# Kernel optimization log

Measured on AMD Instinct MI355X. Metric: run time of the kernel, lower is better.

Reference implementation:

```python
import jax, jax.numpy as jnp
import numpy as np

B, T, C, H = 2048, 81, 128, 4
HD = C // H  # head dim = 32


def sudoku_mask():
    # att[i,j] = 0 if cells i,j share a row, column, or 3x3 block; else -inf.
    idx = np.arange(81)
    row, col = idx // 9, idx % 9
    block_a, block_b = col // 3, row // 3  # equality test matches original's swapped naming
    same = (row[:, None] == row[None, :]) | (col[:, None] == col[None, :]) | (
        (block_a[:, None] == block_a[None, :]) & (block_b[:, None] == block_b[None, :]))
    return jnp.asarray(np.where(same, 0.0, -np.inf), dtype=jnp.float32)


def setup_inputs() -> dict:
    key = jax.random.key(0)
    ks = jax.random.split(key, 7)
    s = 1.0 / np.sqrt(C)
    return {
        "x": jax.random.normal(ks[0], (B, T, C), jnp.float32),
        "key_value_states": jax.random.normal(ks[1], (B, T, C), jnp.float32),
        "Wq": jax.random.normal(ks[2], (C, C), jnp.float32) * s,
        "bq": jnp.zeros((C,), jnp.float32),
        "Wk": jax.random.normal(ks[3], (C, C), jnp.float32) * s,
        "bk": jnp.zeros((C,), jnp.float32),
        "Wv": jax.random.normal(ks[4], (C, C), jnp.float32) * s,
        "bv": jnp.zeros((C,), jnp.float32),
        "Wp": jax.random.normal(ks[5], (C, C), jnp.float32) * s,
        "bp": jnp.zeros((C,), jnp.float32),
    }


def reference(x, key_value_states, Wq, bq, Wk, bk, Wv, bv, Wp, bp):
    mask = sudoku_mask()  # [T, Te]
    # projections -> [B, H, T, HD]
    q = (x @ Wq + bq).reshape(B, T, H, HD).transpose(0, 2, 1, 3)
    k = (key_value_states @ Wk + bk).reshape(B, T, H, HD).transpose(0, 2, 1, 3)
    v = (key_value_states @ Wv + bv).reshape(B, T, H, HD).transpose(0, 2, 1, 3)
    att = jnp.einsum("bhqd,bhkd->bhqk", q, k) * (1.0 / np.sqrt(HD))
    att = att + mask  # broadcast over [B, H]
    att_to_check = att  # pre-softmax scores (the clone in torch)
    p = jax.nn.softmax(att, axis=-1)  # attn_drop is identity (p=0 / eval)
    y = jnp.einsum("bhqk,bhkd->bhqd", p, v)
    y = y.transpose(0, 2, 1, 3).reshape(B, T, C)
    y = y @ Wp + bp  # resid_drop is identity
    return (y, att_to_check)
```

## Files before the change

kernel.cpp:

```cpp
#include <hip/hip_runtime.h>
#include <math.h>

namespace {
constexpr int NB = 2048;
constexpr int TT = 81;
constexpr int CC = 128;
constexpr int NH = 4;
constexpr int HD = 32;
constexpr int BT  = TT * CC;
constexpr int ATTS = NH * TT * TT;
constexpr int MT = NB * TT / 64;
constexpr float SCALE = 0.17677669529663687f;
constexpr float MASKED = -1.0e30f;
}

__device__ __forceinline__ int swz(int row, int k) {
    return row * CC + (k ^ ((row & 7) << 2));
}

struct MaskTab { unsigned w[TT][4]; };
constexpr MaskTab make_mask() {
    MaskTab t{};
    for (int i = 0; i < TT; ++i) {
        const int ri = i / 9, ci = i % 9;
        for (int j = 0; j < TT; ++j) {
            const int rj = j / 9, cj = j % 9;
            const bool same = (ri == rj) || (ci == cj) ||
                              ((ri / 3 == rj / 3) && (ci / 3 == cj / 3));
            if (same) t.w[i][j >> 5] |= 1u << (j & 31);
        }
    }
    return t;
}
__device__ __constant__ MaskTab MASKT = make_mask();

__global__ __launch_bounds__(512, 6)
void qkv_gemm(const float* __restrict__ x, const float* __restrict__ kvs,
              const float* __restrict__ Wq, const float* __restrict__ bq,
              const float* __restrict__ Wk, const float* __restrict__ bk,
              const float* __restrict__ Wv, const float* __restrict__ bv,
              float* __restrict__ qk_region,
              float* __restrict__ v_region,
              size_t qk_stride)
{
    __shared__ float act[64 * CC];

    const int tid = threadIdx.x;
    const int sel = blockIdx.y;
    const float* W    = (sel == 0) ? Wq : (sel == 1) ? Wk : Wv;
    const float* bias = (sel == 0) ? bq : (sel == 1) ? bk : bv;
    const float* src  = (sel == 0) ? x  : kvs;
    const size_t gbase = (size_t)blockIdx.x * 64 * CC;

    for (int t = tid; t < 64 * CC / 4; t += 512) {
        const int row = t >> 5;
        const int k0  = (t & 31) << 2;
        *reinterpret_cast<float4*>(&act[swz(row, k0)]) =
            *reinterpret_cast<const float4*>(src + gbase + t * 4);
    }
    __syncthreads();

    const int lane = tid & 63;
    const int col0 = __builtin_amdgcn_readfirstlane(tid >> 6) << 4;
    const int m    = blockIdx.x * 64 + lane;
    const int bb   = m / TT;
    const int ii   = m - bb * TT;

    float acc[16];
    #pragma unroll
    for (int c = 0; c < 16; ++c) acc[c] = bias[col0 + c];

    for (int k4 = 0; k4 < 32; ++k4) {
        const float4 a = *reinterpret_cast<const float4*>(&act[swz(lane, k4 * 4)]);
        const float* wr = W + (size_t)(k4 * 4) * CC + col0;
        #pragma unroll
        for (int kk = 0; kk < 4; ++kk) {
            const float av = (kk == 0) ? a.x : (kk == 1) ? a.y
                           : (kk == 2) ? a.z : a.w;
            #pragma unroll
            for (int c4 = 0; c4 < 4; ++c4) {
                const float4 w =
                    *reinterpret_cast<const float4*>(wr + kk * CC + c4 * 4);
                acc[c4 * 4 + 0] = fmaf(av, w.x, acc[c4 * 4 + 0]);
                acc[c4 * 4 + 1] = fmaf(av, w.y, acc[c4 * 4 + 1]);
                acc[c4 * 4 + 2] = fmaf(av, w.z, acc[c4 * 4 + 2]);
                acc[c4 * 4 + 3] = fmaf(av, w.w, acc[c4 * 4 + 3]);
            }
        }
    }

    float* dst = (sel == 2)
        ? v_region  + (size_t)bb * BT + ii * CC + col0
        : qk_region + (size_t)bb * qk_stride + (size_t)sel * BT + ii * CC + col0;
    #pragma unroll
    for (int c4 = 0; c4 < 4; ++c4)
        reinterpret_cast<float4*>(dst)[c4] =
            make_float4(acc[c4*4+0], acc[c4*4+1], acc[c4*4+2], acc[c4*4+3]);
}

__global__ __launch_bounds__(256, 3)
void attn_head(const float* __restrict__ qk_ws,
               float* __restrict__ att_region,
               float* __restrict__ yv_region)
{
    __shared__ float Qh[TT * HD];
    __shared__ float Vh[TT * HD];
    __shared__ float Su[TT * TT];

    const int bh  = blockIdx.x;
    const int b   = bh >> 2;
    const int h   = bh & 3;
    const int tid = threadIdx.x;

    const float* qbase = qk_ws + (size_t)b * 2 * BT;
    const float* kbase = qbase + BT;
    float* vbase = yv_region + (size_t)b * BT;
    float* abase = att_region + (size_t)b * ATTS + (size_t)h * TT * TT;

    for (int t = tid; t < TT * 8; t += 256) {
        const int i  = t >> 3;
        const int c4 = (t & 7) << 2;
        const float4 qv = *reinterpret_cast<const float4*>(qbase + i * CC + h * HD + c4);
        const float4 vv = *reinterpret_cast<const float4*>(vbase + i * CC + h * HD + c4);
        const float4 kv = *reinterpret_cast<const float4*>(kbase + i * CC + h * HD + c4);
        *reinterpret_cast<float4*>(&Qh[i * HD + c4]) = qv;
        *reinterpret_cast<float4*>(&Vh[i * HD + c4]) = vv;
        Su[i * 33 + c4 + 0] = kv.x;
        Su[i * 33 + c4 + 1] = kv.y;
        Su[i * 33 + c4 + 2] = kv.z;
        Su[i * 33 + c4 + 3] = kv.w;
    }
    __syncthreads();

    const int io = tid / 41;
    const int jg = tid - io * 41;
    const bool sact = tid < 246;
    const int j0 = jg * 2;
    const int j1 = j0 + 1;
    const bool hasj1 = j1 < TT;
    const int j1r = hasj1 ? j1 : j0;

    float k0[HD], k1[HD];
    if (sact) {
        #pragma unroll
        for (int c = 0; c < HD; ++c) {
            k0[c] = Su[j0 * 33 + c];
            k1[c] = Su[j1r * 33 + c];
        }
    }
    __syncthreads();

    if (sact) {
        const int w0 = j0 >> 5, s0b = j0 & 31;
        const int w1 = j1 >> 5, s1b = j1 & 31;
        const int i0   = (io < 3) ? io * 14 : 42 + (io - 3) * 13;
        const int ilen = (io < 3) ? 14 : 13;
        for (int t = 0; t < ilen; ++t) {
            const int i = i0 + t;
            const float4* qf = reinterpret_cast<const float4*>(&Qh[i * HD]);
            float s0 = 0.f, s1 = 0.f;
            #pragma unroll
            for (int c4 = 0; c4 < 8; ++c4) {
                const float4 q4 = qf[c4];
                s0 = fmaf(q4.x, k0[c4*4+0], s0); s0 = fmaf(q4.y, k0[c4*4+1], s0);
                s0 = fmaf(q4.z, k0[c4*4+2], s0); s0 = fmaf(q4.w, k0[c4*4+3], s0);
                s1 = fmaf(q4.x, k1[c4*4+0], s1); s1 = fmaf(q4.y, k1[c4*4+1], s1);
                s1 = fmaf(q4.z, k1[c4*4+2], s1); s1 = fmaf(q4.w, k1[c4*4+3], s1);
            }
            const unsigned mw0 = MASKT.w[i][w0];
            Su[i * TT + j0] = ((mw0 >> s0b) & 1u) ? s0 * SCALE : MASKED;
            if (hasj1) {
                const unsigned mw1 = MASKT.w[i][w1];
                Su[i * TT + j1] = ((mw1 >> s1b) & 1u) ? s1 * SCALE : MASKED;
            }
        }
    }
    __syncthreads();

    for (int e = tid; e < TT * TT; e += 256)
        abase[e] = Su[e];

    if (tid < 2 * TT) {
        const int ph = tid / TT;
        const int pi = tid - ph * TT;
        const int d0 = ph * 16;
        const float* srow = &Su[pi * TT];

        float m0 = -INFINITY, m1 = -INFINITY, m2 = -INFINITY;
        for (int j = 0; j < TT; j += 3) {
            m0 = fmaxf(m0, srow[j + 0]);
            m1 = fmaxf(m1, srow[j + 1]);
            m2 = fmaxf(m2, srow[j + 2]);
        }
        const float mx = fmaxf(m0, fmaxf(m1, m2));

        float acc[16];
        #pragma unroll
        for (int c = 0; c < 16; ++c) acc[c] = 0.f;
        float sum = 0.f;
        for (int j = 0; j < TT; ++j) {
            const float e = __expf(srow[j] - mx);
            sum += e;
            const float4* vr = reinterpret_cast<const float4*>(&Vh[j * HD + d0]);
            #pragma unroll
            for (int c4 = 0; c4 < 4; ++c4) {
                const float4 v4 = vr[c4];
                acc[c4 * 4 + 0] = fmaf(e, v4.x, acc[c4 * 4 + 0]);
                acc[c4 * 4 + 1] = fmaf(e, v4.y, acc[c4 * 4 + 1]);
                acc[c4 * 4 + 2] = fmaf(e, v4.z, acc[c4 * 4 + 2]);
                acc[c4 * 4 + 3] = fmaf(e, v4.w, acc[c4 * 4 + 3]);
            }
        }
        const float inv = 1.0f / sum;
        float* dst = vbase + pi * CC + h * HD + d0;
        #pragma unroll
        for (int c4 = 0; c4 < 4; ++c4)
            reinterpret_cast<float4*>(dst)[c4] =
                make_float4(acc[c4*4+0]*inv, acc[c4*4+1]*inv,
                            acc[c4*4+2]*inv, acc[c4*4+3]*inv);
    }
}

__global__ __launch_bounds__(1024, 4)
void attn_fused(float* __restrict__ att_region, float* __restrict__ yv_region)
{
    __shared__ float Kl[TT * CC];
    __shared__ float Vl[TT * CC];
    __shared__ float scmp[NH * TT * 21];
    __shared__ signed char slotT[TT * TT];

    const int b   = blockIdx.x;
    const int tid = threadIdx.x;
    float* abase = att_region + (size_t)b * ATTS;
    float* vbase = yv_region  + (size_t)b * BT;

    if (tid < TT) {
        const int i = tid, ri = i / 9, ci = i - ri * 9;
        int cnt = 0;
        for (int j = 0; j < TT; ++j) {
            const int rj = j / 9, cj = j - rj * 9;
            const bool same = (ri == rj) | (ci == cj) |
                              ((ri / 3 == rj / 3) & (ci / 3 == cj / 3));
            slotT[i * TT + j] = same ? (signed char)(cnt++) : (signed char)(-1);
        }
    }
    for (int t = tid; t < BT / 4; t += 1024) {
        reinterpret_cast<float4*>(Kl)[t] =
            reinterpret_cast<const float4*>(abase + BT)[t];
        reinterpret_cast<float4*>(Vl)[t] =
            reinterpret_cast<const float4*>(vbase)[t];
    }
    __syncthreads();

    const int p = tid;
    int h = 0, half = 0, i = 0;
    if (p < 2 * NH * TT) {
        h = p / (2 * TT);
        const int rem = p - h * 2 * TT;
        half = rem / TT;
        i = rem - half * TT;
    }

    if (p < 2 * NH * TT) {
        float q[HD];
        const float* qr = abase + i * CC + h * HD;
        #pragma unroll
        for (int c4 = 0; c4 < 8; ++c4) {
            const float4 t4 = *reinterpret_cast<const float4*>(qr + c4 * 4);
            q[c4*4+0] = t4.x; q[c4*4+1] = t4.y; q[c4*4+2] = t4.z; q[c4*4+3] = t4.w;
        }
        const signed char* srow = &slotT[i * TT];
        const int rbase = (h * TT + i) * 21;
        const int j0 = half ? 41 : 0;
        const int j1 = half ? TT : 41;
        for (int j = j0; j < j1; ++j) {
            const float* kr = &Kl[j * CC + h * HD];
            float p0 = 0.f, p1 = 0.f, p2 = 0.f, p3 = 0.f;
            #pragma unroll
            for (int c4 = 0; c4 < 8; c4 += 4) {
                const float4 k0 = *reinterpret_cast<const float4*>(kr + (c4+0)*4);
                const float4 k1 = *reinterpret_cast<const float4*>(kr + (c4+1)*4);
                const float4 k2 = *reinterpret_cast<const float4*>(kr + (c4+2)*4);
                const float4 k3 = *reinterpret_cast<const float4*>(kr + (c4+3)*4);
                p0 = fmaf(q[c4*4+ 0], k0.x, p0); p0 = fmaf(q[c4*4+ 1], k0.y, p0);
                p0 = fmaf(q[c4*4+ 2], k0.z, p0); p0 = fmaf(q[c4*4+ 3], k0.w, p0);
                p1 = fmaf(q[c4*4+ 4], k1.x, p1); p1 = fmaf(q[c4*4+ 5], k1.y, p1);
                p1 = fmaf(q[c4*4+ 6], k1.z, p1); p1 = fmaf(q[c4*4+ 7], k1.w, p1);
                p2 = fmaf(q[c4*4+ 8], k2.x, p2); p2 = fmaf(q[c4*4+ 9], k2.y, p2);
                p2 = fmaf(q[c4*4+10], k2.z, p2); p2 = fmaf(q[c4*4+11], k2.w, p2);
                p3 = fmaf(q[c4*4+12], k3.x, p3); p3 = fmaf(q[c4*4+13], k3.y, p3);
                p3 = fmaf(q[c4*4+14], k3.z, p3); p3 = fmaf(q[c4*4+15], k3.w, p3);
            }
            const float s = ((p0 + p1) + (p2 + p3)) * SCALE;
            const int sl = srow[j];
            if (sl >= 0) scmp[rbase + sl] = s;
        }
    }
    __syncthreads();

    for (int e4 = tid; e4 < ATTS / 4; e4 += 1024) {
        float4 o;
        float* op = reinterpret_cast<float*>(&o);
        #pragma unroll
        for (int u = 0; u < 4; ++u) {
            const int e   = e4 * 4 + u;
            const int row = e / TT;
            const int j   = e - row * TT;
            const int i2  = row - (row / TT) * TT;
            const int sl  = slotT[i2 * TT + j];
            op[u] = (sl >= 0) ? scmp[row * 21 + sl] : MASKED;
        }
        reinterpret_cast<float4*>(abase)[e4] = o;
    }

    if (p < 2 * NH * TT) {
        const int rbase = (h * TT + i) * 21;
        const int dim0  = h * HD + half * 16;
        float mx = -INFINITY;
        #pragma unroll
        for (int s = 0; s < 21; ++s) mx = fmaxf(mx, scmp[rbase + s]);

        float acc[16];
        #pragma unroll
        for (int c = 0; c < 16; ++c) acc[c] = 0.f;
        float sum = 0.f;
        const signed char* srow = &slotT[i * TT];
        for (int j = 0; j < TT; ++j) {
            const int sl  = srow[j];
            const int sli = sl < 0 ? 0 : sl;
            const float sv = scmp[rbase + sli];
            const float e  = (sl >= 0) ? __expf(sv - mx) : 0.0f;
            sum += e;
            const float* vr = &Vl[j * CC + dim0];
            #pragma unroll
            for (int c4 = 0; c4 < 4; ++c4) {
                const float4 v4 = *reinterpret_cast<const float4*>(vr + c4 * 4);
                acc[c4*4+0] = fmaf(e, v4.x, acc[c4*4+0]);
                acc[c4*4+1] = fmaf(e, v4.y, acc[c4*4+1]);
                acc[c4*4+2] = fmaf(e, v4.z, acc[c4*4+2]);
                acc[c4*4+3] = fmaf(e, v4.w, acc[c4*4+3]);
            }
        }
        const float inv = 1.0f / sum;
        float* dst = vbase + i * CC + dim0;
        #pragma unroll
        for (int c4 = 0; c4 < 4; ++c4)
            reinterpret_cast<float4*>(dst)[c4] =
                make_float4(acc[c4*4+0]*inv, acc[c4*4+1]*inv,
                            acc[c4*4+2]*inv, acc[c4*4+3]*inv);
    }
}

__global__ __launch_bounds__(512, 8)
void out_gemm(float* __restrict__ y_region,
              const float* __restrict__ Wp, const float* __restrict__ bp)
{
    __shared__ float yl[64 * CC];

    const int tid = threadIdx.x;
    const size_t gbase = (size_t)blockIdx.x * 64 * CC;

    for (int t = tid; t < 64 * CC / 4; t += 512) {
        const int row = t >> 5;
        const int k0  = (t & 31) << 2;
        *reinterpret_cast<float4*>(&yl[swz(row, k0)]) =
            *reinterpret_cast<const float4*>(y_region + gbase + t * 4);
    }
    __syncthreads();

    const int lane = tid & 63;
    const int col0 = __builtin_amdgcn_readfirstlane(tid >> 6) << 4;

    float acc[16];
    #pragma unroll
    for (int c = 0; c < 16; ++c) acc[c] = bp[col0 + c];

    for (int k4 = 0; k4 < 32; ++k4) {
        const float4 a = *reinterpret_cast<const float4*>(&yl[swz(lane, k4 * 4)]);
        const float* wr = Wp + (size_t)(k4 * 4) * CC + col0;
        #pragma unroll
        for (int kk = 0; kk < 4; ++kk) {
            const float av = (kk == 0) ? a.x : (kk == 1) ? a.y
                           : (kk == 2) ? a.z : a.w;
            #pragma unroll
            for (int c4 = 0; c4 < 4; ++c4) {
                const float4 w =
                    *reinterpret_cast<const float4*>(wr + kk * CC + c4 * 4);
                acc[c4*4+0] = fmaf(av, w.x, acc[c4*4+0]);
                acc[c4*4+1] = fmaf(av, w.y, acc[c4*4+1]);
                acc[c4*4+2] = fmaf(av, w.z, acc[c4*4+2]);
                acc[c4*4+3] = fmaf(av, w.w, acc[c4*4+3]);
            }
        }
    }

    float* dst = y_region + gbase + lane * CC + col0;
    #pragma unroll
    for (int c4 = 0; c4 < 4; ++c4)
        reinterpret_cast<float4*>(dst)[c4] =
            make_float4(acc[c4*4+0], acc[c4*4+1], acc[c4*4+2], acc[c4*4+3]);
}

extern "C" void kernel_launch(void* const* d_in, const int* in_sizes, int n_in,
                              void* d_out, int out_size, void* d_ws, size_t ws_size,
                              hipStream_t stream) {
    (void)in_sizes; (void)n_in; (void)out_size;
    const float* x   = (const float*)d_in[0];
    const float* kvs = (const float*)d_in[1];
    const float* Wq  = (const float*)d_in[2];
    const float* bq  = (const float*)d_in[3];
    const float* Wk  = (const float*)d_in[4];
    const float* bk  = (const float*)d_in[5];
    const float* Wv  = (const float*)d_in[6];
    const float* bv  = (const float*)d_in[7];
    const float* Wp  = (const float*)d_in[8];
    const float* bp  = (const float*)d_in[9];

    float* ybase   = (float*)d_out;
    float* attbase = ybase + (size_t)NB * BT;

    const size_t need = (size_t)NB * 2 * BT * sizeof(float);
    if (ws_size >= need) {
        float* qkws = (float*)d_ws;
        qkv_gemm<<<dim3(MT, 3), 512, 0, stream>>>(x, kvs, Wq, bq, Wk, bk, Wv, bv,
                                                  qkws, ybase, (size_t)(2 * BT));
        attn_head<<<NB * NH, 256, 0, stream>>>(qkws, attbase, ybase);
    } else {
        qkv_gemm<<<dim3(MT, 3), 512, 0, stream>>>(x, kvs, Wq, bq, Wk, bk, Wv, bv,
                                                  attbase, ybase, (size_t)ATTS);
        attn_fused<<<NB, 1024, 0, stream>>>(attbase, ybase);
    }
    out_gemm<<<MT, 512, 0, stream>>>(ybase, Wp, bp);
}
```

Before: 526.5 us.

## Run QKV projection on bf16 MFMA with three-way split precision emulation

Replaces the FP32 scalar QKV GEMM with a matrix-core kernel that splits activations and weights into high/mid/low bf16 parts. Six MFMA products per k-group approximate FP32 accuracy. A small prep kernel transposes and splits the weights into workspace each call. The goal is to move GEMM arithmetic onto the MFMA units, at the cost of extra split work, more LDS, an extra launch, and scattered scalar output stores.

Result: slower. 803.7 us (+52.6%).

```diff
diff --git a/kernel.cpp b/kernel.cpp
--- a/kernel.cpp
+++ b/kernel.cpp
@@ -1,4 +1,5 @@
 #include <hip/hip_runtime.h>
+#include <hip/hip_bf16.h>
 #include <math.h>
 
 namespace {
@@ -12,6 +13,20 @@
 constexpr int MT = NB * TT / 64;
 constexpr float SCALE = 0.17677669529663687f;
 constexpr float MASKED = -1.0e30f;
+constexpr int WPLANE = 128 * 128;
+}
+
+typedef short           bf16x8 __attribute__((ext_vector_type(8)));
+typedef float           f32x4  __attribute__((ext_vector_type(4)));
+typedef unsigned short  u16x8  __attribute__((ext_vector_type(8)));
+
+__device__ __forceinline__ unsigned short bf16_of(float f) {
+    __hip_bfloat16 h = __float2bfloat16(f);
+    return *reinterpret_cast<unsigned short*>(&h);
+}
+__device__ __forceinline__ float f_of_bf16(unsigned short u) {
+    __hip_bfloat16 h = *reinterpret_cast<__hip_bfloat16*>(&u);
+    return __bfloat162float(h);
 }
 
 __device__ __forceinline__ int swz(int row, int k) {
@@ -34,13 +49,131 @@
 }
 __device__ __constant__ MaskTab MASKT = make_mask();
 
+__global__ __launch_bounds__(256, 8)
+void wprep(const float* __restrict__ Wq, const float* __restrict__ Wk,
+           const float* __restrict__ Wv, const float* __restrict__ Wp,
+           unsigned short* __restrict__ wt)
+{
+    const int mi = blockIdx.y;
+    const float* W = (mi == 0) ? Wq : (mi == 1) ? Wk : (mi == 2) ? Wv : Wp;
+    const int e = blockIdx.x * 256 + threadIdx.x;
+    const int n = e >> 7, k = e & 127;
+    const float w = W[k * CC + n];
+    const unsigned short hb = bf16_of(w);
+    const float r1 = w - f_of_bf16(hb);
+    const unsigned short mb = bf16_of(r1);
+    const unsigned short lb = bf16_of(r1 - f_of_bf16(mb));
+    unsigned short* base = wt + mi * 3 * WPLANE;
+    base[e]              = hb;
+    base[WPLANE + e]     = mb;
+    base[2 * WPLANE + e] = lb;
+}
+
+__global__ __launch_bounds__(256, 3)
+void qkv_mfma(const float* __restrict__ x, const float* __restrict__ kvs,
+              const float* __restrict__ bq, const float* __restrict__ bk,
+              const float* __restrict__ bv,
+              const unsigned short* __restrict__ wt,
+              float* __restrict__ qk_region,
+              float* __restrict__ v_region)
+{
+    __shared__ unsigned short Ph[64 * CC];
+    __shared__ unsigned short Pm[64 * CC];
+    __shared__ unsigned short Pl[64 * CC];
+
+    const int tid = threadIdx.x;
+    const int sel = blockIdx.y;
+    const float* src  = (sel == 0) ? x  : kvs;
+    const float* bias = (sel == 0) ? bq : (sel == 1) ? bk : bv;
+    const size_t gbase = (size_t)blockIdx.x * 64 * CC;
+
+    for (int t = tid; t < 1024; t += 256) {
+        const int row = t >> 4, gi = t & 15;
+        const float* s = src + gbase + row * CC + gi * 8;
+        float v[8];
+        *reinterpret_cast<float4*>(&v[0]) = *reinterpret_cast<const float4*>(s);
+        *reinterpret_cast<float4*>(&v[4]) = *reinterpret_cast<const float4*>(s + 4);
+        u16x8 h8, m8, l8;
+        #pragma unroll
+        for (int e = 0; e < 8; ++e) {
+            const float f = v[e];
+            const unsigned short hb = bf16_of(f);
+            const float r1 = f - f_of_bf16(hb);
+            const unsigned short mb = bf16_of(r1);
+            const unsigned short lb = bf16_of(r1 - f_of_bf16(mb));
+            h8[e] = hb; m8[e] = mb; l8[e] = lb;
+        }
+        const int idx = row * CC + ((gi ^ (row & 15)) << 3);
+        *reinterpret_cast<u16x8*>(&Ph[idx]) = h8;
+        *reinterpret_cast<u16x8*>(&Pm[idx]) = m8;
+        *reinterpret_cast<u16x8*>(&Pl[idx]) = l8;
+    }
+    __syncthreads();
+
+    const int wid  = tid >> 6;
+    const int lane = tid & 63;
+    const int lr   = lane & 15;
+    const int lg   = lane >> 4;
+    const unsigned short* wh = wt + sel * 3 * WPLANE;
+    const unsigned short* wm = wh + WPLANE;
+    const unsigned short* wl = wh + 2 * WPLANE;
+
+    for (int cgi = 0; cgi < 2; ++cgi) {
+        const int cg  = wid * 2 + cgi;
+        const int col = cg * 16 + lr;
+
+        bf16x8 Bh[4], Bm[4], Bl[4];
+        #pragma unroll
+        for (int kg = 0; kg < 4; ++kg) {
+            const int off = col * CC + kg * 32 + lg * 8;
+            Bh[kg] = *reinterpret_cast<const bf16x8*>(wh + off);
+            Bm[kg] = *reinterpret_cast<const bf16x8*>(wm + off);
+            Bl[kg] = *reinterpret_cast<const bf16x8*>(wl + off);
+        }
+        const float bcol = bias[col];
+
+        #pragma unroll
+        for (int rg = 0; rg < 4; ++rg) {
+            const int r = rg * 16 + lr;
+            bf16x8 Fh[4], Fm[4], Fl[4];
+            #pragma unroll
+            for (int kg = 0; kg < 4; ++kg) {
+                const int idx = r * CC + (((kg * 4 + lg) ^ lr) << 3);
+                Fh[kg] = *reinterpret_cast<const bf16x8*>(&Ph[idx]);
+                Fm[kg] = *reinterpret_cast<const bf16x8*>(&Pm[idx]);
+                Fl[kg] = *reinterpret_cast<const bf16x8*>(&Pl[idx]);
+            }
+            f32x4 acc = {bcol, bcol, bcol, bcol};
+            #pragma unroll
+            for (int kg = 0; kg < 4; ++kg) {
+                acc = __builtin_amdgcn_mfma_f32_16x16x32_bf16(Fh[kg], Bh[kg], acc, 0, 0, 0);
+                acc = __builtin_amdgcn_mfma_f32_16x16x32_bf16(Fh[kg], Bm[kg], acc, 0, 0, 0);
+                acc = __builtin_amdgcn_mfma_f32_16x16x32_bf16(Fm[kg], Bh[kg], acc, 0, 0, 0);
+                acc = __builtin_amdgcn_mfma_f32_16x16x32_bf16(Fh[kg], Bl[kg], acc, 0, 0, 0);
+                acc = __builtin_amdgcn_mfma_f32_16x16x32_bf16(Fl[kg], Bh[kg], acc, 0, 0, 0);
+                acc = __builtin_amdgcn_mfma_f32_16x16x32_bf16(Fm[kg], Bm[kg], acc, 0, 0, 0);
+            }
+            const int mbase = blockIdx.x * 64 + rg * 16 + lg * 4;
+            #pragma unroll
+            for (int p = 0; p < 4; ++p) {
+                const int m  = mbase + p;
+                const int bb = m / TT;
+                const int ii = m - bb * TT;
+                float* dst = (sel == 2)
+                    ? v_region  + (size_t)bb * BT + ii * CC + col
+                    : qk_region + (size_t)bb * (2 * BT) + (size_t)sel * BT + ii * CC + col;
+                *dst = acc[p];
+            }
+        }
+    }
+}
+
 __global__ __launch_bounds__(512, 6)
 void qkv_gemm(const float* __restrict__ x, const float* __restrict__ kvs,
               const float* __restrict__ Wq, const float* __restrict__ bq,
               const float* __restrict__ Wk, const float* __restrict__ bk,
               const float* __restrict__ Wv, const float* __restrict__ bv,
-              float* __restrict__ qk_region,
-              float* __restrict__ v_region,
+              float* __restrict__ qk_region, float* __restrict__ v_region,
               size_t qk_stride)
 {
     __shared__ float act[64 * CC];
@@ -419,11 +552,14 @@
     float* ybase   = (float*)d_out;
     float* attbase = ybase + (size_t)NB * BT;
 
-    const size_t need = (size_t)NB * 2 * BT * sizeof(float);
-    if (ws_size >= need) {
+    const size_t qk_bytes = (size_t)NB * 2 * BT * sizeof(float);
+    const size_t wt_bytes = (size_t)4 * 3 * WPLANE * sizeof(unsigned short);
+    if (ws_size >= qk_bytes + wt_bytes) {
         float* qkws = (float*)d_ws;
-        qkv_gemm<<<dim3(MT, 3), 512, 0, stream>>>(x, kvs, Wq, bq, Wk, bk, Wv, bv,
-                                                  qkws, ybase, (size_t)(2 * BT));
+        unsigned short* wt = (unsigned short*)((char*)d_ws + qk_bytes);
+        wprep<<<dim3(64, 4), 256, 0, stream>>>(Wq, Wk, Wv, Wp, wt);
+        qkv_mfma<<<dim3(MT, 3), 256, 0, stream>>>(x, kvs, bq, bk, bv, wt,
+                                                  qkws, ybase);
         attn_head<<<NB * NH, 256, 0, stream>>>(qkws, attbase, ybase);
     } else {
         qkv_gemm<<<dim3(MT, 3), 512, 0, stream>>>(x, kvs, Wq, bq, Wk, bk, Wv, bv,
```
